# Kernel optimization log

Hardware: AMD Instinct MI355X
Metric: run time of the kernel (lower is better)

The kernel has to match this reference:

```python
import jax, jax.numpy as jnp
import numpy as np

B, F0, D = 4096, 39, 16
CROSS_LAYER_SIZE = (128, 128)


def _he_uniform(key, shape):
    fan_in = int(np.prod(shape[:-1]))
    limit = np.sqrt(6.0 / fan_in)
    return jax.random.uniform(key, shape, jnp.float32, -limit, limit)


def setup_inputs() -> dict:
    key = jax.random.key(0)
    k_x, k_f0, k_f1, k_w, k_b = jax.random.split(key, 5)
    x = jax.random.normal(k_x, (B, F0, D), dtype=jnp.float32)
    # field_nums with direct=False: [39, 128//2=64, 64]
    f0 = _he_uniform(k_f0, (F0 * F0, CROSS_LAYER_SIZE[0]))          # (1521, 128)
    f1 = _he_uniform(k_f1, (F0 * (CROSS_LAYER_SIZE[0] // 2), CROSS_LAYER_SIZE[1]))  # (2496, 128)
    out_dim = CROSS_LAYER_SIZE[0] // 2 + CROSS_LAYER_SIZE[1]        # 192
    dense_w = _he_uniform(k_w, (out_dim, 1))
    dense_b = jnp.zeros((1,), dtype=jnp.float32)
    return {"x": x, "f0": f0, "f1": f1, "dense_w": dense_w, "dense_b": dense_b}


def reference(x, f0, f1, dense_w, dense_b):
    # CIN forward (direct=False, use_bias=False, use_residual=False, relu)
    # x: (B, F0, D)
    filters = [f0, f1]
    n_layers = len(CROSS_LAYER_SIZE)
    h = x  # hidden state, (B, Fk, D)
    finals = []
    for idx, L in enumerate(CROSS_LAYER_SIZE):
        Fk = h.shape[1]
        # filter f_ has shape (F0*Fk, L) with i (field of x0) major, j (field of h) minor
        Wr = filters[idx].reshape(F0, Fk, L)
        # fused outer product + conv1d (kernel width 1 == matmul over i,j):
        # z[b, m, d] = sum_{i,j} x[b,i,d] * h[b,j,d] * W[i,j,m]
        z = jnp.einsum('bid,bjd,ijm->bmd', x, h, Wr)  # (B, L, D)
        z = jax.nn.relu(z)
        if idx != n_layers - 1:
            # split along feature-map axis: first half feeds next layer,
            # second half goes to output
            h = z[:, : L // 2, :]
            finals.append(z[:, L // 2:, :])
        else:
            finals.append(z)
    result = jnp.sum(jnp.concatenate(finals, axis=1), axis=-1)  # (B, 192)
    return result @ dense_w + dense_b  # (B, 1)
```

## Files before the change

### kernel.cpp

```cpp
#include <hip/hip_runtime.h>


typedef _Float16 h2    __attribute__((ext_vector_type(2)));
typedef _Float16 f16x8 __attribute__((ext_vector_type(8)));
typedef __attribute__((ext_vector_type(16))) float f32x16;

#define XBB 1160
#define L0C 30
#define NCH 110

__device__ __constant__ int IG0[L0C] = {0,0,0,0,0, 1,1,1,1,1, 2,2,2,2, 3,3,3,3, 4,4,4, 5,5,5, 6,6, 7,7, 8, 9};
__device__ __constant__ int JG0[L0C] = {0,1,2,3,4, 0,1,2,3,4, 1,2,3,4, 1,2,3,4, 2,3,4, 2,3,4, 3,4, 3,4, 4, 4};
#define IG0T(c) ((c)<5?0:(c)<10?1:(c)<14?2:(c)<18?3:(c)<21?4:(c)<24?5:(c)<26?6:(c)<28?7:(c)<29?8:9)
#define JG0T(c) ((c)<10?((c)%5):(c)<18?(((c)-10)%4+1):(c)<24?(((c)-18)%3+2):(c)<28?(((c)-24)%2+3):4)

__global__ __launch_bounds__(256)
void CIN_repack(const float* __restrict__ f0, const float* __restrict__ f1,
                uint4* __restrict__ ws)
{
    const int tid  = blockIdx.x * 256 + threadIdx.x;
    const int n    = tid & 127;
    const int slot = tid >> 7;
    const int half = slot & 1;
    const int kh   = (slot >> 1) & 1;
    const int ch   = slot >> 2;
    float v[8];
    if (ch < L0C) {
        const int ig = IG0[ch], jg = JG0[ch];
        const int i = ig * 4 + kh * 2 + half;
#pragma unroll
        for (int t = 0; t < 8; ++t) {
            const int j = jg * 8 + t;
            float val = 0.f;
            if (i < 39 && j < 39 && j >= i) {
                val = f0[(i * 39 + j) * 128 + n];
                if (j > i) val += f0[(j * 39 + i) * 128 + n];
            }
            v[t] = val;
        }
    } else {
        const int c1 = ch - L0C;
        const int jg = c1 / 5, ig = c1 - jg * 5;
        const int j = jg * 4 + kh * 2 + half;
#pragma unroll
        for (int t = 0; t < 8; ++t) {
            const int i = ig * 8 + t;
            v[t] = (i < 39) ? f1[(i * 64 + j) * 128 + n] : 0.f;
        }
    }
    union { h2 h[4]; uint4 q; } pk;
#pragma unroll
    for (int t = 0; t < 4; ++t)
        pk.h[t] = h2{(_Float16)v[2 * t], (_Float16)v[2 * t + 1]};
    const int lane = half * 32 + (n & 31);
    const int cg   = n >> 5;
    ws[ch * 512 + kh * 256 + cg * 64 + lane] = pk.q;
}

__global__ __launch_bounds__(256, 2)
void CIN_main(const float* __restrict__ x,
              const char* __restrict__ wsB,
              const float* __restrict__ dw,
              const float* __restrict__ db,
              float* __restrict__ out)
{
    __shared__ __align__(16) _Float16 xsH[4 * XBB];
    __shared__ __align__(4)  _Float16 hsH[4][64][18];
    __shared__ float dws[192];
    __shared__ float red[4][4];

    const int tid  = threadIdx.x;
    const int w    = tid >> 6;
    const int lane = tid & 63;
    const int half = lane >> 5;
    const int d    = lane & 15;
    const int bsel = (lane >> 4) & 1;
    const int col  = lane & 31;

    const char* wbase = wsB + lane * 16 + w * 1024 + 2048;
    f16x8 Bb[4][2];
    auto loadBg = [&](int ch, f16x8 (&B)[2]) {
        const char* p0 = wbase + (size_t)ch * 8192;
        B[0] = *(const f16x8*)(p0 - 2048);
        B[1] = *(const f16x8*)(p0 + 2048);
    };

    loadBg(0, Bb[0]);
    loadBg(1, Bb[1]);
    loadBg(2, Bb[2]);
    loadBg(3, Bb[3]);

    const float4* xg4 = (const float4*)(x + (size_t)blockIdx.x * 4 * 624);
    for (int e4 = tid; e4 < 624; e4 += 256) {
        float4 v = xg4[e4];
        int bb = e4 / 156, r = e4 - bb * 156;
        int i = r >> 2, d0 = (r & 3) * 4;
        _Float16* bp = xsH + bb * XBB + i;
        bp[(d0 + 0) * 72] = (_Float16)v.x; bp[(d0 + 1) * 72] = (_Float16)v.y;
        bp[(d0 + 2) * 72] = (_Float16)v.z; bp[(d0 + 3) * 72] = (_Float16)v.w;
    }
    if (tid < 64) { int bb = tid >> 4, dd = tid & 15; xsH[bb * XBB + dd * 72 + 39] = (_Float16)0.f; }
    if (tid < 192) dws[tid] = dw[tid];
    __syncthreads();

    const _Float16* xrow[2] = {
        xsH + (0 * 2 + bsel) * XBB + d * 72,
        xsH + (1 * 2 + bsel) * XBB + d * 72
    };

    h2 xw[2][20];
#pragma unroll
    for (int p = 0; p < 2; ++p)
#pragma unroll
        for (int w5 = 0; w5 < 5; ++w5) {
            union { f16x8 v; h2 h[4]; } u;
            u.v = *(const f16x8*)(xrow[p] + w5 * 8);
#pragma unroll
            for (int q = 0; q < 4; ++q) xw[p][w5 * 4 + q] = u.h[q];
        }

    f32x16 acc[2];
#pragma unroll
    for (int p = 0; p < 2; ++p)
#pragma unroll
        for (int r = 0; r < 16; ++r) acc[p][r] = 0.f;

    h2 sp2[2][2];

#pragma unroll
    for (int c = 0; c < L0C; ++c) {
        const int ig = IG0T(c);
        const int jg = JG0T(c);
        if ((c == 0) || (IG0T(c) != IG0T(c - 1))) {
#pragma unroll
            for (int p = 0; p < 2; ++p)
#pragma unroll
                for (int kh = 0; kh < 2; ++kh) {
                    const h2 pr = xw[p][ig * 2 + kh];
                    const _Float16 vv = half ? pr.y : pr.x;
                    sp2[p][kh] = h2{vv, vv};
                }
        }
#pragma unroll
        for (int p = 0; p < 2; ++p) {
            union { h2 h[4]; f16x8 v; } a0, a1;
#pragma unroll
            for (int q = 0; q < 4; ++q) {
                a0.h[q] = sp2[p][0] * xw[p][jg * 4 + q];
                a1.h[q] = sp2[p][1] * xw[p][jg * 4 + q];
            }
            acc[p] = __builtin_amdgcn_mfma_f32_32x32x16_f16(a0.v, Bb[c & 3][0], acc[p], 0, 0, 0);
            acc[p] = __builtin_amdgcn_mfma_f32_32x32x16_f16(a1.v, Bb[c & 3][1], acc[p], 0, 0, 0);
        }
        loadBg(c + 4, Bb[c & 3]);
    }

    float cs[4] = {0.f, 0.f, 0.f, 0.f};
    if (w < 2) {
#pragma unroll
        for (int p = 0; p < 2; ++p)
#pragma unroll
            for (int r = 0; r < 16; r += 2) {
                const int row = (r & 3) + 8 * (r >> 2) + 4 * half;
                h2 pr = h2{(_Float16)fmaxf(acc[p][r],     0.f),
                           (_Float16)fmaxf(acc[p][r + 1], 0.f)};
                *(h2*)&hsH[p * 2 + (row >> 4)][w * 32 + col][row & 15] = pr;
            }
    } else {
        const float dwv = dws[(w - 2) * 32 + col];
#pragma unroll
        for (int p = 0; p < 2; ++p)
#pragma unroll
            for (int r = 0; r < 16; ++r) {
                const int row = (r & 3) + 8 * (r >> 2) + 4 * half;
                cs[p * 2 + (row >> 4)] += fmaxf(acc[p][r], 0.f) * dwv;
            }
    }
#pragma unroll
    for (int p = 0; p < 2; ++p)
#pragma unroll
        for (int r = 0; r < 16; ++r) acc[p][r] = 0.f;
    __syncthreads();

#pragma unroll 1
    for (int o2 = 0; o2 < 4; ++o2) {
#pragma unroll
        for (int u = 0; u < 20; ++u) {
            const int ig2 = u % 5;
            if (ig2 == 0) {
                const int jb = (o2 * 4 + u / 5) * 4;
#pragma unroll
                for (int p = 0; p < 2; ++p)
#pragma unroll
                    for (int kh = 0; kh < 2; ++kh) {
                        const _Float16 s = hsH[p * 2 + bsel][jb + kh * 2 + half][d];
                        sp2[p][kh] = h2{s, s};
                    }
            }
#pragma unroll
            for (int p = 0; p < 2; ++p) {
                union { h2 h[4]; f16x8 v; } a0, a1;
#pragma unroll
                for (int q = 0; q < 4; ++q) {
                    a0.h[q] = sp2[p][0] * xw[p][ig2 * 4 + q];
                    a1.h[q] = sp2[p][1] * xw[p][ig2 * 4 + q];
                }
                acc[p] = __builtin_amdgcn_mfma_f32_32x32x16_f16(a0.v, Bb[(2 + u) & 3][0], acc[p], 0, 0, 0);
                acc[p] = __builtin_amdgcn_mfma_f32_32x32x16_f16(a1.v, Bb[(2 + u) & 3][1], acc[p], 0, 0, 0);
            }
            int chn = 30 + o2 * 20 + u + 4; if (chn > NCH - 1) chn = NCH - 1;
            loadBg(chn, Bb[(2 + u) & 3]);
        }
    }

    {
        const float dwv = dws[64 + w * 32 + col];
#pragma unroll
        for (int p = 0; p < 2; ++p)
#pragma unroll
            for (int r = 0; r < 16; ++r) {
                const int row = (r & 3) + 8 * (r >> 2) + 4 * half;
                cs[p * 2 + (row >> 4)] += fmaxf(acc[p][r], 0.f) * dwv;
            }
    }
#pragma unroll
    for (int rr = 0; rr < 4; ++rr)
#pragma unroll
        for (int off = 32; off > 0; off >>= 1)
            cs[rr] += __shfl_xor(cs[rr], off, 64);
    if (lane == 0) {
#pragma unroll
        for (int rr = 0; rr < 4; ++rr) red[w][rr] = cs[rr];
    }
    __syncthreads();
    if (tid < 4)
        out[blockIdx.x * 4 + tid] = red[0][tid] + red[1][tid] + red[2][tid] + red[3][tid] + db[0];
}

extern "C" void kernel_launch(void* const* d_in, const int* in_sizes, int n_in,
                              void* d_out, int out_size, void* d_ws, size_t ws_size,
                              hipStream_t stream)
{
    const float* x  = (const float*)d_in[0];
    const float* f0 = (const float*)d_in[1];
    const float* f1 = (const float*)d_in[2];
    const float* dw = (const float*)d_in[3];
    const float* db = (const float*)d_in[4];
    float* out = (float*)d_out;

    CIN_repack<<<dim3(220), dim3(256), 0, stream>>>(f0, f1, (uint4*)d_ws);
    CIN_main<<<dim3(1024), dim3(256), 0, stream>>>(x, (const char*)d_ws, dw, db, out);
}
```

Baseline: 125.4 us.

## Retile CIN main kernel so each wave covers two batch pairs and two N-quarters

Each block now handles 8 batch rows instead of 4. The four waves are split as 2 batch-pairs by 2 column-halves, so each wave computes two 32-column N tiles and reuses each A operand across both. Per-wave weight loads now cover 64 columns with double buffering (depth 2 instead of 4), and the grid is halved. This targets B-fragment global/L2 traffic per batch row, at the cost of more accumulator registers and shallower prefetch.

After: 121.0 us. 1.04x faster.

```diff
diff --git a/kernel.cpp b/kernel.cpp
--- a/kernel.cpp
+++ b/kernel.cpp
@@ -64,34 +64,36 @@
               const float* __restrict__ db,
               float* __restrict__ out)
 {
-    __shared__ __align__(16) _Float16 xsH[4 * XBB];
-    __shared__ __align__(4)  _Float16 hsH[4][64][18];
+    __shared__ __align__(16) _Float16 xsH[8 * XBB];
+    __shared__ __align__(4)  _Float16 hsH[8][64][18];
     __shared__ float dws[192];
     __shared__ float red[4][4];
 
     const int tid  = threadIdx.x;
     const int w    = tid >> 6;
+    const int wp   = w >> 1;
+    const int wn   = w & 1;
     const int lane = tid & 63;
     const int half = lane >> 5;
     const int d    = lane & 15;
     const int bsel = (lane >> 4) & 1;
     const int col  = lane & 31;
 
-    const char* wbase = wsB + lane * 16 + w * 1024 + 2048;
-    f16x8 Bb[4][2];
-    auto loadBg = [&](int ch, f16x8 (&B)[2]) {
+    const char* wbase = wsB + lane * 16 + wn * 2048 + 2560;
+    f16x8 Bb[2][2][2];
+    auto loadBg = [&](int ch, f16x8 (&B)[2][2]) {
         const char* p0 = wbase + (size_t)ch * 8192;
-        B[0] = *(const f16x8*)(p0 - 2048);
-        B[1] = *(const f16x8*)(p0 + 2048);
+        B[0][0] = *(const f16x8*)(p0 - 2560);
+        B[0][1] = *(const f16x8*)(p0 - 1536);
+        B[1][0] = *(const f16x8*)(p0 + 1536);
+        B[1][1] = *(const f16x8*)(p0 + 2560);
     };
 
     loadBg(0, Bb[0]);
     loadBg(1, Bb[1]);
-    loadBg(2, Bb[2]);
-    loadBg(3, Bb[3]);
-
-    const float4* xg4 = (const float4*)(x + (size_t)blockIdx.x * 4 * 624);
-    for (int e4 = tid; e4 < 624; e4 += 256) {
+
+    const float4* xg4 = (const float4*)(x + (size_t)blockIdx.x * 8 * 624);
+    for (int e4 = tid; e4 < 1248; e4 += 256) {
         float4 v = xg4[e4];
         int bb = e4 / 156, r = e4 - bb * 156;
         int i = r >> 2, d0 = (r & 3) * 4;
@@ -99,13 +101,13 @@
         bp[(d0 + 0) * 72] = (_Float16)v.x; bp[(d0 + 1) * 72] = (_Float16)v.y;
         bp[(d0 + 2) * 72] = (_Float16)v.z; bp[(d0 + 3) * 72] = (_Float16)v.w;
     }
-    if (tid < 64) { int bb = tid >> 4, dd = tid & 15; xsH[bb * XBB + dd * 72 + 39] = (_Float16)0.f; }
+    if (tid < 128) { int bb = tid >> 4, dd = tid & 15; xsH[bb * XBB + dd * 72 + 39] = (_Float16)0.f; }
     if (tid < 192) dws[tid] = dw[tid];
     __syncthreads();
 
     const _Float16* xrow[2] = {
-        xsH + (0 * 2 + bsel) * XBB + d * 72,
-        xsH + (1 * 2 + bsel) * XBB + d * 72
+        xsH + ((wp * 2 + 0) * 2 + bsel) * XBB + d * 72,
+        xsH + ((wp * 2 + 1) * 2 + bsel) * XBB + d * 72
     };
 
     h2 xw[2][20];
@@ -119,11 +121,13 @@
             for (int q = 0; q < 4; ++q) xw[p][w5 * 4 + q] = u.h[q];
         }
 
-    f32x16 acc[2];
+    f32x16 acc[2][2];
 #pragma unroll
     for (int p = 0; p < 2; ++p)
 #pragma unroll
-        for (int r = 0; r < 16; ++r) acc[p][r] = 0.f;
+        for (int nq = 0; nq < 2; ++nq)
+#pragma unroll
+            for (int r = 0; r < 16; ++r) acc[p][nq][r] = 0.f;
 
     h2 sp2[2][2];
 
@@ -149,37 +153,46 @@
                 a0.h[q] = sp2[p][0] * xw[p][jg * 4 + q];
                 a1.h[q] = sp2[p][1] * xw[p][jg * 4 + q];
             }
-            acc[p] = __builtin_amdgcn_mfma_f32_32x32x16_f16(a0.v, Bb[c & 3][0], acc[p], 0, 0, 0);
-            acc[p] = __builtin_amdgcn_mfma_f32_32x32x16_f16(a1.v, Bb[c & 3][1], acc[p], 0, 0, 0);
-        }
-        loadBg(c + 4, Bb[c & 3]);
+            acc[p][0] = __builtin_amdgcn_mfma_f32_32x32x16_f16(a0.v, Bb[c & 1][0][0], acc[p][0], 0, 0, 0);
+            acc[p][1] = __builtin_amdgcn_mfma_f32_32x32x16_f16(a0.v, Bb[c & 1][0][1], acc[p][1], 0, 0, 0);
+            acc[p][0] = __builtin_amdgcn_mfma_f32_32x32x16_f16(a1.v, Bb[c & 1][1][0], acc[p][0], 0, 0, 0);
+            acc[p][1] = __builtin_amdgcn_mfma_f32_32x32x16_f16(a1.v, Bb[c & 1][1][1], acc[p][1], 0, 0, 0);
+        }
+        loadBg(c + 2, Bb[c & 1]);
     }
 
     float cs[4] = {0.f, 0.f, 0.f, 0.f};
-    if (w < 2) {
+    if (wn == 0) {
 #pragma unroll
         for (int p = 0; p < 2; ++p)
 #pragma unroll
-            for (int r = 0; r < 16; r += 2) {
-                const int row = (r & 3) + 8 * (r >> 2) + 4 * half;
-                h2 pr = h2{(_Float16)fmaxf(acc[p][r],     0.f),
-                           (_Float16)fmaxf(acc[p][r + 1], 0.f)};
-                *(h2*)&hsH[p * 2 + (row >> 4)][w * 32 + col][row & 15] = pr;
-            }
+            for (int nq = 0; nq < 2; ++nq)
+#pragma unroll
+                for (int r = 0; r < 16; r += 2) {
+                    const int row = (r & 3) + 8 * (r >> 2) + 4 * half;
+                    h2 pr = h2{(_Float16)fmaxf(acc[p][nq][r],     0.f),
+                               (_Float16)fmaxf(acc[p][nq][r + 1], 0.f)};
+                    *(h2*)&hsH[(wp * 2 + p) * 2 + (row >> 4)][nq * 32 + col][row & 15] = pr;
+                }
     } else {
-        const float dwv = dws[(w - 2) * 32 + col];
-#pragma unroll
-        for (int p = 0; p < 2; ++p)
-#pragma unroll
-            for (int r = 0; r < 16; ++r) {
-                const int row = (r & 3) + 8 * (r >> 2) + 4 * half;
-                cs[p * 2 + (row >> 4)] += fmaxf(acc[p][r], 0.f) * dwv;
-            }
+#pragma unroll
+        for (int nq = 0; nq < 2; ++nq) {
+            const float dwv = dws[nq * 32 + col];
+#pragma unroll
+            for (int p = 0; p < 2; ++p)
+#pragma unroll
+                for (int r = 0; r < 16; ++r) {
+                    const int row = (r & 3) + 8 * (r >> 2) + 4 * half;
+                    cs[p * 2 + (row >> 4)] += fmaxf(acc[p][nq][r], 0.f) * dwv;
+                }
+        }
     }
 #pragma unroll
     for (int p = 0; p < 2; ++p)
 #pragma unroll
-        for (int r = 0; r < 16; ++r) acc[p][r] = 0.f;
+        for (int nq = 0; nq < 2; ++nq)
+#pragma unroll
+            for (int r = 0; r < 16; ++r) acc[p][nq][r] = 0.f;
     __syncthreads();
 
 #pragma unroll 1
@@ -193,7 +206,7 @@
                 for (int p = 0; p < 2; ++p)
 #pragma unroll
                     for (int kh = 0; kh < 2; ++kh) {
-                        const _Float16 s = hsH[p * 2 + bsel][jb + kh * 2 + half][d];
+                        const _Float16 s = hsH[(wp * 2 + p) * 2 + bsel][jb + kh * 2 + half][d];
                         sp2[p][kh] = h2{s, s};
                     }
             }
@@ -205,22 +218,25 @@
                     a0.h[q] = sp2[p][0] * xw[p][ig2 * 4 + q];
                     a1.h[q] = sp2[p][1] * xw[p][ig2 * 4 + q];
                 }
-                acc[p] = __builtin_amdgcn_mfma_f32_32x32x16_f16(a0.v, Bb[(2 + u) & 3][0], acc[p], 0, 0, 0);
-                acc[p] = __builtin_amdgcn_mfma_f32_32x32x16_f16(a1.v, Bb[(2 + u) & 3][1], acc[p], 0, 0, 0);
-            }
-            int chn = 30 + o2 * 20 + u + 4; if (chn > NCH - 1) chn = NCH - 1;
-            loadBg(chn, Bb[(2 + u) & 3]);
-        }
-    }
-
-    {
-        const float dwv = dws[64 + w * 32 + col];
+                acc[p][0] = __builtin_amdgcn_mfma_f32_32x32x16_f16(a0.v, Bb[u & 1][0][0], acc[p][0], 0, 0, 0);
+                acc[p][1] = __builtin_amdgcn_mfma_f32_32x32x16_f16(a0.v, Bb[u & 1][0][1], acc[p][1], 0, 0, 0);
+                acc[p][0] = __builtin_amdgcn_mfma_f32_32x32x16_f16(a1.v, Bb[u & 1][1][0], acc[p][0], 0, 0, 0);
+                acc[p][1] = __builtin_amdgcn_mfma_f32_32x32x16_f16(a1.v, Bb[u & 1][1][1], acc[p][1], 0, 0, 0);
+            }
+            int chn = 30 + o2 * 20 + u + 2; if (chn > NCH - 1) chn = NCH - 1;
+            loadBg(chn, Bb[u & 1]);
+        }
+    }
+
+#pragma unroll
+    for (int nq = 0; nq < 2; ++nq) {
+        const float dwv = dws[64 + (wn * 2 + nq) * 32 + col];
 #pragma unroll
         for (int p = 0; p < 2; ++p)
 #pragma unroll
             for (int r = 0; r < 16; ++r) {
                 const int row = (r & 3) + 8 * (r >> 2) + 4 * half;
-                cs[p * 2 + (row >> 4)] += fmaxf(acc[p][r], 0.f) * dwv;
+                cs[p * 2 + (row >> 4)] += fmaxf(acc[p][nq][r], 0.f) * dwv;
             }
     }
 #pragma unroll
@@ -233,8 +249,10 @@
         for (int rr = 0; rr < 4; ++rr) red[w][rr] = cs[rr];
     }
     __syncthreads();
-    if (tid < 4)
-        out[blockIdx.x * 4 + tid] = red[0][tid] + red[1][tid] + red[2][tid] + red[3][tid] + db[0];
+    if (tid < 8) {
+        const int wpp = tid >> 2, l = tid & 3;
+        out[blockIdx.x * 8 + tid] = red[wpp * 2][l] + red[wpp * 2 + 1][l] + db[0];
+    }
 }
 
 extern "C" void kernel_launch(void* const* d_in, const int* in_sizes, int n_in,
@@ -249,5 +267,5 @@
     float* out = (float*)d_out;
 
     CIN_repack<<<dim3(220), dim3(256), 0, stream>>>(f0, f1, (uint4*)d_ws);
-    CIN_main<<<dim3(1024), dim3(256), 0, stream>>>(x, (const char*)d_ws, dw, db, out);
+    CIN_main<<<dim3(512), dim3(256), 0, stream>>>(x, (const char*)d_ws, dw, db, out);
 }
```
